# Kernel optimization log

Measured on AMD Instinct MI355X. Metric: run time of the kernel, lower is better.

## Reference

```python
import jax, jax.numpy as jnp
import numpy as np

N_NODES = 50000
N_EDGES = 800000
IN_DIM = 128
OUT_DIM = 256


def setup_inputs() -> dict:
    key = jax.random.key(0)
    k1, k2, k3, k4 = jax.random.split(key, 4)
    feat = jax.random.normal(k1, (N_NODES, IN_DIM), dtype=jnp.float32)
    # xavier_uniform with relu gain, shape [in_dim, out_dim] (applied as h @ W)
    gain = np.sqrt(2.0)
    bound = gain * np.sqrt(6.0 / (IN_DIM + OUT_DIM))
    W = jax.random.uniform(k2, (IN_DIM, OUT_DIM), dtype=jnp.float32,
                           minval=-bound, maxval=bound)
    src = jax.random.randint(k3, (N_EDGES,), 0, N_NODES, dtype=jnp.int64)
    dst = jax.random.randint(k4, (N_EDGES,), 0, N_NODES, dtype=jnp.int64)
    return {"feat": feat, "W": W, "src": src, "dst": dst}


def reference(feat, W, src, dst):
    n = feat.shape[0]
    # mean aggregation over incoming neighbors (copy_src + mean on dst)
    msg_sum = jax.ops.segment_sum(feat[src], dst, num_segments=n)  # [N, in_dim]
    deg = jax.ops.segment_sum(jnp.ones_like(dst, dtype=feat.dtype), dst,
                              num_segments=n)  # [N]
    h_neigh = msg_sum / jnp.maximum(deg, 1.0)[:, None]  # zero-degree -> 0
    # self_loop=False path: fc((feat + h_neigh) / 2), then relu
    h = ((feat + h_neigh) * 0.5) @ W  # [N, out_dim]
    return jax.nn.relu(h)
```

## Files before the change

kernel.cpp:

```cpp
#include <hip/hip_runtime.h>
#include <hip/hip_fp16.h>

#define N_NODES 50000
#define N_EDGES 800000
#define IN_DIM  128
#define OUT_DIM 256
#define SCAN_BLOCKS ((N_NODES + 255) / 256)
#define WT_STRIDE 136

typedef _Float16 f16x8 __attribute__((ext_vector_type(8)));
typedef float f32x4 __attribute__((ext_vector_type(4)));

__device__ __forceinline__ int detect_i64(const int* __restrict__ idx) {
  int orv = 0;
#pragma unroll
  for (int j = 1; j < 32; j += 2) orv |= idx[j];
  return orv == 0;
}

__global__ __launch_bounds__(256) void hist_cast(
    const int* __restrict__ dst, const float* __restrict__ feat,
    __half* __restrict__ feat16, int* __restrict__ hist,
    int* __restrict__ slot) {
  const int f = detect_i64(dst);
  const int e = blockIdx.x * 256 + threadIdx.x;
  const int d = dst[f ? 2 * (long)e : (long)e];
  slot[e] = atomicAdd(&hist[d], 1);

  if (feat16 != nullptr) {
    size_t i = (size_t)e * 8;
    float4 v0 = *reinterpret_cast<const float4*>(feat + i);
    float4 v1 = *reinterpret_cast<const float4*>(feat + i + 4);
    __half2 h[4];
    h[0] = __floats2half2_rn(v0.x, v0.y);
    h[1] = __floats2half2_rn(v0.z, v0.w);
    h[2] = __floats2half2_rn(v1.x, v1.y);
    h[3] = __floats2half2_rn(v1.z, v1.w);
    *reinterpret_cast<float4*>(feat16 + i) = *reinterpret_cast<float4*>(h);
  }
}

__global__ __launch_bounds__(256) void scan_block(
    const int* __restrict__ hist, int* __restrict__ row_start,
    int* __restrict__ bsum, const float* __restrict__ W,
    __half* __restrict__ WT16g) {
  __shared__ int s[256];
  int tid = threadIdx.x;
  int i = blockIdx.x * 256 + tid;
  int v = (i < N_NODES) ? hist[i] : 0;
  s[tid] = v;
  __syncthreads();
  for (int off = 1; off < 256; off <<= 1) {
    int t = (tid >= off) ? s[tid - off] : 0;
    __syncthreads();
    s[tid] += t;
    __syncthreads();
  }
  if (i < N_NODES) row_start[i] = s[tid] - v;
  if (tid == 255) bsum[blockIdx.x] = s[255];

  if (blockIdx.x < 128) {
    int n = 2 * blockIdx.x + (tid >> 7);
    int k = tid & 127;
    WT16g[n * IN_DIM + k] = __float2half(W[k * OUT_DIM + n]);
  }
}

__global__ __launch_bounds__(256) void scan_add(
    const int* __restrict__ bsum, int* __restrict__ row_start) {
  __shared__ int sb[256];
  int tid = threadIdx.x;
  sb[tid] = (tid < (int)blockIdx.x) ? bsum[tid] : 0;
  __syncthreads();
  for (int off = 128; off > 0; off >>= 1) {
    if (tid < off) sb[tid] += sb[tid + off];
    __syncthreads();
  }
  int i = blockIdx.x * 256 + tid;
  if (i < N_NODES) row_start[i] += sb[0];
  if (i == 0) row_start[N_NODES] = N_EDGES;
}

__global__ __launch_bounds__(256) void scatter_kernel(
    const int* __restrict__ src, const int* __restrict__ dst,
    const int* __restrict__ row_start, const int* __restrict__ slot,
    int* __restrict__ esrc) {
  const int f = detect_i64(src);
  const int t = blockIdx.x * 256 + threadIdx.x;
  if (t >= N_EDGES / 2) return;
  int s0, s1, d0, d1;
  if (f) {
    int4 sv = *reinterpret_cast<const int4*>(src + 4 * (long)t);
    int4 dv = *reinterpret_cast<const int4*>(dst + 4 * (long)t);
    s0 = sv.x; s1 = sv.z; d0 = dv.x; d1 = dv.z;
  } else {
    int2 sv = *reinterpret_cast<const int2*>(src + 2 * (long)t);
    int2 dv = *reinterpret_cast<const int2*>(dst + 2 * (long)t);
    s0 = sv.x; s1 = sv.y; d0 = dv.x; d1 = dv.y;
  }
  int2 sl = *reinterpret_cast<const int2*>(slot + 2 * (long)t);
  esrc[row_start[d0] + sl.x] = s0;
  esrc[row_start[d1] + sl.y] = s1;
}

__global__ __launch_bounds__(256) void aggregate_f16(
    const float* __restrict__ feat, const __half* __restrict__ feat16,
    const int* __restrict__ esrc, const int* __restrict__ row_start,
    __half2* __restrict__ x) {
  int node = blockIdx.x * 4 + ((int)threadIdx.x >> 6);
  int lane = (int)threadIdx.x & 63;
  if (node >= N_NODES) return;
  int rs = row_start[node];
  int re = row_start[node + 1];
  float2 a0 = {0.f, 0.f}, a1 = {0.f, 0.f}, a2 = {0.f, 0.f}, a3 = {0.f, 0.f};
  int e = rs;
  for (; e + 3 < re; e += 4) {
    int s0 = esrc[e + 0];
    int s1 = esrc[e + 1];
    int s2 = esrc[e + 2];
    int s3 = esrc[e + 3];
    float2 v0 = __half22float2(*reinterpret_cast<const __half2*>(
        feat16 + (size_t)s0 * IN_DIM + lane * 2));
    float2 v1 = __half22float2(*reinterpret_cast<const __half2*>(
        feat16 + (size_t)s1 * IN_DIM + lane * 2));
    float2 v2 = __half22float2(*reinterpret_cast<const __half2*>(
        feat16 + (size_t)s2 * IN_DIM + lane * 2));
    float2 v3 = __half22float2(*reinterpret_cast<const __half2*>(
        feat16 + (size_t)s3 * IN_DIM + lane * 2));
    a0.x += v0.x; a0.y += v0.y;
    a1.x += v1.x; a1.y += v1.y;
    a2.x += v2.x; a2.y += v2.y;
    a3.x += v3.x; a3.y += v3.y;
  }
  for (; e < re; ++e) {
    float2 v0 = __half22float2(*reinterpret_cast<const __half2*>(
        feat16 + (size_t)esrc[e] * IN_DIM + lane * 2));
    a0.x += v0.x; a0.y += v0.y;
  }
  float deg = (float)(re - rs);
  float rdeg = (deg > 0.f) ? 1.0f / deg : 0.0f;
  float2 f = *reinterpret_cast<const float2*>(
      feat + (size_t)node * IN_DIM + lane * 2);
  float x0 = (f.x + ((a0.x + a1.x) + (a2.x + a3.x)) * rdeg) * 0.5f;
  float x1 = (f.y + ((a0.y + a1.y) + (a2.y + a3.y)) * rdeg) * 0.5f;
  x[(size_t)node * (IN_DIM / 2) + lane] = __floats2half2_rn(x0, x1);
}

__global__ __launch_bounds__(256) void aggregate_f32(
    const float* __restrict__ feat, const int* __restrict__ esrc,
    const int* __restrict__ row_start, __half2* __restrict__ x) {
  int node = blockIdx.x * 4 + ((int)threadIdx.x >> 6);
  int lane = (int)threadIdx.x & 63;
  if (node >= N_NODES) return;
  int rs = row_start[node];
  int re = row_start[node + 1];
  float2 a0 = {0.f, 0.f}, a1 = {0.f, 0.f};
  int e = rs;
  for (; e + 1 < re; e += 2) {
    float2 v0 = *reinterpret_cast<const float2*>(
        feat + (size_t)esrc[e] * IN_DIM + lane * 2);
    float2 v1 = *reinterpret_cast<const float2*>(
        feat + (size_t)esrc[e + 1] * IN_DIM + lane * 2);
    a0.x += v0.x; a0.y += v0.y;
    a1.x += v1.x; a1.y += v1.y;
  }
  if (e < re) {
    float2 v0 = *reinterpret_cast<const float2*>(
        feat + (size_t)esrc[e] * IN_DIM + lane * 2);
    a0.x += v0.x; a0.y += v0.y;
  }
  float deg = (float)(re - rs);
  float rdeg = (deg > 0.f) ? 1.0f / deg : 0.0f;
  float2 f = *reinterpret_cast<const float2*>(
      feat + (size_t)node * IN_DIM + lane * 2);
  float x0 = (f.x + (a0.x + a1.x) * rdeg) * 0.5f;
  float x1 = (f.y + (a0.y + a1.y) * rdeg) * 0.5f;
  x[(size_t)node * (IN_DIM / 2) + lane] = __floats2half2_rn(x0, x1);
}

__global__ __launch_bounds__(256) void mfma_gemm(
    const _Float16* __restrict__ x, const __half* __restrict__ WT16g,
    float* __restrict__ out) {
  __shared__ _Float16 WT[OUT_DIM * WT_STRIDE];

  const int tid = threadIdx.x;
#pragma unroll
  for (int i = 0; i < 16; ++i) {
    int c = i * 256 + tid;
    int n = c >> 4;
    int kc = c & 15;
    *reinterpret_cast<float4*>(&WT[n * WT_STRIDE + kc * 8]) =
        *reinterpret_cast<const float4*>(WT16g + c * 8);
  }
  __syncthreads();

  const int wave = tid >> 6;
  const int lane = tid & 63;
  const int m = lane & 15;
  const int g = lane >> 4;
  const long row_base = (long)blockIdx.x * 128 + wave * 32;

  f16x8 a[2][4];
#pragma unroll
  for (int rt = 0; rt < 2; ++rt) {
    long row = row_base + rt * 16 + m;
#pragma unroll
    for (int kt = 0; kt < 4; ++kt) {
      if (row < N_NODES) {
        a[rt][kt] = *reinterpret_cast<const f16x8*>(
            x + row * IN_DIM + kt * 32 + g * 8);
      } else {
        a[rt][kt] = f16x8{};
      }
    }
  }

#pragma unroll
  for (int nt = 0; nt < 16; ++nt) {
    f16x8 b[4];
#pragma unroll
    for (int kt = 0; kt < 4; ++kt) {
      b[kt] = *reinterpret_cast<const f16x8*>(
          &WT[(nt * 16 + m) * WT_STRIDE + kt * 32 + g * 8]);
    }
    f32x4 acc0 = {0.f, 0.f, 0.f, 0.f};
    f32x4 acc1 = {0.f, 0.f, 0.f, 0.f};
#pragma unroll
    for (int kt = 0; kt < 4; ++kt) {
      acc0 = __builtin_amdgcn_mfma_f32_16x16x32_f16(a[0][kt], b[kt], acc0, 0, 0, 0);
      acc1 = __builtin_amdgcn_mfma_f32_16x16x32_f16(a[1][kt], b[kt], acc1, 0, 0, 0);
    }
    const int col = nt * 16 + m;
#pragma unroll
    for (int j = 0; j < 4; ++j) {
      long r0 = row_base + g * 4 + j;
      long r1 = row_base + 16 + g * 4 + j;
      if (r0 < N_NODES)
        __builtin_nontemporal_store(fmaxf(acc0[j], 0.f),
                                    &out[r0 * OUT_DIM + col]);
      if (r1 < N_NODES)
        __builtin_nontemporal_store(fmaxf(acc1[j], 0.f),
                                    &out[r1 * OUT_DIM + col]);
    }
  }
}

extern "C" void kernel_launch(void* const* d_in, const int* in_sizes, int n_in,
                              void* d_out, int out_size, void* d_ws,
                              size_t ws_size, hipStream_t stream) {
  const float* feat = (const float*)d_in[0];
  const float* W = (const float*)d_in[1];
  const int* src = (const int*)d_in[2];
  const int* dst = (const int*)d_in[3];
  float* out = (float*)d_out;

  char* p = (char*)d_ws;
  __half* x = (__half*)p;    p += (size_t)N_NODES * IN_DIM * 2;
  int* slot = (int*)x;
  int* esrc = (int*)p;       p += (size_t)N_EDGES * 4;
  int* hist = (int*)p;       p += (size_t)N_NODES * 4;
  int* row_start = (int*)p;  p += (size_t)(N_NODES + 1) * 4;
  int* bsum = (int*)p;       p += 256 * 4;
  p = (char*)(((uintptr_t)p + 15) & ~(uintptr_t)15);
  __half* WT16g = (__half*)p; p += (size_t)OUT_DIM * IN_DIM * 2;
  __half* feat16 = (__half*)p;
  size_t need_f16 =
      ((char*)feat16 - (char*)d_ws) + (size_t)N_NODES * IN_DIM * 2;
  const bool f16_path = (ws_size >= need_f16);

  hipMemsetAsync(hist, 0, (size_t)N_NODES * 4, stream);

  const int eblocks = N_EDGES / 256;
  hist_cast<<<eblocks, 256, 0, stream>>>(dst, feat,
                                         f16_path ? feat16 : nullptr, hist,
                                         slot);
  scan_block<<<SCAN_BLOCKS, 256, 0, stream>>>(hist, row_start, bsum, W, WT16g);
  scan_add<<<SCAN_BLOCKS, 256, 0, stream>>>(bsum, row_start);
  scatter_kernel<<<(N_EDGES / 2 + 255) / 256, 256, 0, stream>>>(
      src, dst, row_start, slot, esrc);
  if (f16_path) {
    aggregate_f16<<<(N_NODES + 3) / 4, 256, 0, stream>>>(feat, feat16, esrc,
                                                         row_start,
                                                         (__half2*)x);
  } else {
    aggregate_f32<<<(N_NODES + 3) / 4, 256, 0, stream>>>(feat, esrc, row_start,
                                                         (__half2*)x);
  }
  mfma_gemm<<<(N_NODES + 127) / 128, 256, 0, stream>>>(
      (const _Float16*)x, WT16g, out);
}
```

Baseline: 201.1 us.

## Fuse CSR build stages into one persistent kernel with grid barriers

Replaces the histogram/cast, two-pass scan and scatter kernels with a single persistent 1024-block kernel that uses software grid barriers between phases. The block scan is redone over 49 nodes per block so each block handles its own slice. The aim is to remove several kernel launch gaps and drain points. It also drops the fp32 fallback aggregation path. The grid barrier relies on all 1024 blocks being co-resident, which can deadlock if occupancy is lower, and spinning barriers add their own latency.

```diff
diff --git a/kernel.cpp b/kernel.cpp
--- a/kernel.cpp
+++ b/kernel.cpp
@@ -5,8 +5,9 @@
 #define N_EDGES 800000
 #define IN_DIM  128
 #define OUT_DIM 256
-#define SCAN_BLOCKS ((N_NODES + 255) / 256)
 #define WT_STRIDE 136
+#define NBLK 1024
+#define NODES_PER_BLK 49
 
 typedef _Float16 f16x8 __attribute__((ext_vector_type(8)));
 typedef float f32x4 __attribute__((ext_vector_type(4)));
@@ -18,17 +19,42 @@
   return orv == 0;
 }
 
-__global__ __launch_bounds__(256) void hist_cast(
-    const int* __restrict__ dst, const float* __restrict__ feat,
-    __half* __restrict__ feat16, int* __restrict__ hist,
-    int* __restrict__ slot) {
-  const int f = detect_i64(dst);
-  const int e = blockIdx.x * 256 + threadIdx.x;
-  const int d = dst[f ? 2 * (long)e : (long)e];
-  slot[e] = atomicAdd(&hist[d], 1);
-
-  if (feat16 != nullptr) {
-    size_t i = (size_t)e * 8;
+__device__ __forceinline__ void grid_barrier(int* counter, int* gen) {
+  __syncthreads();
+  if (threadIdx.x == 0) {
+    __threadfence();
+    int g = __hip_atomic_load(gen, __ATOMIC_RELAXED, __HIP_MEMORY_SCOPE_AGENT);
+    int prev = __hip_atomic_fetch_add(counter, 1, __ATOMIC_ACQ_REL,
+                                      __HIP_MEMORY_SCOPE_AGENT);
+    if (prev == NBLK - 1) {
+      __hip_atomic_store(counter, 0, __ATOMIC_RELAXED,
+                         __HIP_MEMORY_SCOPE_AGENT);
+      __hip_atomic_store(gen, g + 1, __ATOMIC_RELEASE,
+                         __HIP_MEMORY_SCOPE_AGENT);
+    } else {
+      while (__hip_atomic_load(gen, __ATOMIC_ACQUIRE,
+                               __HIP_MEMORY_SCOPE_AGENT) == g) {
+        __builtin_amdgcn_s_sleep(2);
+      }
+    }
+  }
+  __syncthreads();
+}
+
+__global__ __launch_bounds__(256, 4) void mega_csr(
+    const float* __restrict__ feat, const float* __restrict__ W,
+    const int* __restrict__ src, const int* __restrict__ dst,
+    __half* __restrict__ feat16, __half* __restrict__ WT16g,
+    int* __restrict__ hist, int* __restrict__ slot,
+    int* __restrict__ row_start, int* __restrict__ bsum,
+    int* __restrict__ esrc, int* __restrict__ bar) {
+  const int tid = threadIdx.x;
+  const int b = blockIdx.x;
+  const int gtid = b * 256 + tid;
+  const int fd = detect_i64(dst);
+
+  for (int t = gtid; t < (N_NODES * IN_DIM) / 8; t += NBLK * 256) {
+    size_t i = (size_t)t * 8;
     float4 v0 = *reinterpret_cast<const float4*>(feat + i);
     float4 v1 = *reinterpret_cast<const float4*>(feat + i + 4);
     __half2 h[4];
@@ -38,69 +64,70 @@
     h[3] = __floats2half2_rn(v1.z, v1.w);
     *reinterpret_cast<float4*>(feat16 + i) = *reinterpret_cast<float4*>(h);
   }
-}
-
-__global__ __launch_bounds__(256) void scan_block(
-    const int* __restrict__ hist, int* __restrict__ row_start,
-    int* __restrict__ bsum, const float* __restrict__ W,
-    __half* __restrict__ WT16g) {
-  __shared__ int s[256];
-  int tid = threadIdx.x;
-  int i = blockIdx.x * 256 + tid;
-  int v = (i < N_NODES) ? hist[i] : 0;
-  s[tid] = v;
-  __syncthreads();
-  for (int off = 1; off < 256; off <<= 1) {
-    int t = (tid >= off) ? s[tid - off] : 0;
+  if (gtid < OUT_DIM * IN_DIM) {
+    int k = gtid & (IN_DIM - 1);
+    int n = gtid >> 7;
+    WT16g[gtid] = __float2half(W[k * OUT_DIM + n]);
+  }
+  for (int e = gtid; e < N_EDGES; e += NBLK * 256) {
+    int d = dst[fd ? 2 * (long)e : (long)e];
+    slot[e] = atomicAdd(&hist[d], 1);
+  }
+
+  grid_barrier(bar, bar + 1);
+
+  __shared__ int s[64];
+  __shared__ int sb[256];
+  int v = 0;
+  if (tid < 64) {
+    int node = b * NODES_PER_BLK + tid;
+    v = (tid < NODES_PER_BLK && node < N_NODES) ? hist[node] : 0;
+    s[tid] = v;
+  }
+  __syncthreads();
+  for (int off = 1; off < 64; off <<= 1) {
+    int t2 = (tid < 64 && tid >= off) ? s[tid - off] : 0;
     __syncthreads();
-    s[tid] += t;
+    if (tid < 64) s[tid] += t2;
     __syncthreads();
   }
-  if (i < N_NODES) row_start[i] = s[tid] - v;
-  if (tid == 255) bsum[blockIdx.x] = s[255];
-
-  if (blockIdx.x < 128) {
-    int n = 2 * blockIdx.x + (tid >> 7);
-    int k = tid & 127;
-    WT16g[n * IN_DIM + k] = __float2half(W[k * OUT_DIM + n]);
-  }
-}
-
-__global__ __launch_bounds__(256) void scan_add(
-    const int* __restrict__ bsum, int* __restrict__ row_start) {
-  __shared__ int sb[256];
-  int tid = threadIdx.x;
-  sb[tid] = (tid < (int)blockIdx.x) ? bsum[tid] : 0;
+  if (tid == 0) bsum[b] = s[NODES_PER_BLK - 1];
+
+  grid_barrier(bar, bar + 1);
+
+  int part = 0;
+  for (int i = tid; i < b; i += 256) part += bsum[i];
+  sb[tid] = part;
   __syncthreads();
   for (int off = 128; off > 0; off >>= 1) {
     if (tid < off) sb[tid] += sb[tid + off];
     __syncthreads();
   }
-  int i = blockIdx.x * 256 + tid;
-  if (i < N_NODES) row_start[i] += sb[0];
-  if (i == 0) row_start[N_NODES] = N_EDGES;
-}
-
-__global__ __launch_bounds__(256) void scatter_kernel(
-    const int* __restrict__ src, const int* __restrict__ dst,
-    const int* __restrict__ row_start, const int* __restrict__ slot,
-    int* __restrict__ esrc) {
-  const int f = detect_i64(src);
-  const int t = blockIdx.x * 256 + threadIdx.x;
-  if (t >= N_EDGES / 2) return;
-  int s0, s1, d0, d1;
-  if (f) {
-    int4 sv = *reinterpret_cast<const int4*>(src + 4 * (long)t);
-    int4 dv = *reinterpret_cast<const int4*>(dst + 4 * (long)t);
-    s0 = sv.x; s1 = sv.z; d0 = dv.x; d1 = dv.z;
-  } else {
-    int2 sv = *reinterpret_cast<const int2*>(src + 2 * (long)t);
-    int2 dv = *reinterpret_cast<const int2*>(dst + 2 * (long)t);
-    s0 = sv.x; s1 = sv.y; d0 = dv.x; d1 = dv.y;
-  }
-  int2 sl = *reinterpret_cast<const int2*>(slot + 2 * (long)t);
-  esrc[row_start[d0] + sl.x] = s0;
-  esrc[row_start[d1] + sl.y] = s1;
+  int offset = sb[0];
+  if (tid < NODES_PER_BLK) {
+    int node = b * NODES_PER_BLK + tid;
+    if (node < N_NODES) row_start[node] = (s[tid] - v) + offset;
+  }
+  if (gtid == 0) row_start[N_NODES] = N_EDGES;
+
+  grid_barrier(bar, bar + 1);
+
+  const int fs = detect_i64(src);
+  for (int t = gtid; t < N_EDGES / 2; t += NBLK * 256) {
+    int s0, s1, d0, d1;
+    if (fs) {
+      int4 sv = *reinterpret_cast<const int4*>(src + 4 * (long)t);
+      int4 dv = *reinterpret_cast<const int4*>(dst + 4 * (long)t);
+      s0 = sv.x; s1 = sv.z; d0 = dv.x; d1 = dv.z;
+    } else {
+      int2 sv = *reinterpret_cast<const int2*>(src + 2 * (long)t);
+      int2 dv = *reinterpret_cast<const int2*>(dst + 2 * (long)t);
+      s0 = sv.x; s1 = sv.y; d0 = dv.x; d1 = dv.y;
+    }
+    int2 sl = *reinterpret_cast<const int2*>(slot + 2 * (long)t);
+    esrc[row_start[d0] + sl.x] = s0;
+    esrc[row_start[d1] + sl.y] = s1;
+  }
 }
 
 __global__ __launch_bounds__(256) void aggregate_f16(
@@ -146,38 +173,6 @@
   x[(size_t)node * (IN_DIM / 2) + lane] = __floats2half2_rn(x0, x1);
 }
 
-__global__ __launch_bounds__(256) void aggregate_f32(
-    const float* __restrict__ feat, const int* __restrict__ esrc,
-    const int* __restrict__ row_start, __half2* __restrict__ x) {
-  int node = blockIdx.x * 4 + ((int)threadIdx.x >> 6);
-  int lane = (int)threadIdx.x & 63;
-  if (node >= N_NODES) return;
-  int rs = row_start[node];
-  int re = row_start[node + 1];
-  float2 a0 = {0.f, 0.f}, a1 = {0.f, 0.f};
-  int e = rs;
-  for (; e + 1 < re; e += 2) {
-    float2 v0 = *reinterpret_cast<const float2*>(
-        feat + (size_t)esrc[e] * IN_DIM + lane * 2);
-    float2 v1 = *reinterpret_cast<const float2*>(
-        feat + (size_t)esrc[e + 1] * IN_DIM + lane * 2);
-    a0.x += v0.x; a0.y += v0.y;
-    a1.x += v1.x; a1.y += v1.y;
-  }
-  if (e < re) {
-    float2 v0 = *reinterpret_cast<const float2*>(
-        feat + (size_t)esrc[e] * IN_DIM + lane * 2);
-    a0.x += v0.x; a0.y += v0.y;
-  }
-  float deg = (float)(re - rs);
-  float rdeg = (deg > 0.f) ? 1.0f / deg : 0.0f;
-  float2 f = *reinterpret_cast<const float2*>(
-      feat + (size_t)node * IN_DIM + lane * 2);
-  float x0 = (f.x + (a0.x + a1.x) * rdeg) * 0.5f;
-  float x1 = (f.y + (a0.y + a1.y) * rdeg) * 0.5f;
-  x[(size_t)node * (IN_DIM / 2) + lane] = __floats2half2_rn(x0, x1);
-}
-
 __global__ __launch_bounds__(256) void mfma_gemm(
     const _Float16* __restrict__ x, const __half* __restrict__ WT16g,
     float* __restrict__ out) {
@@ -217,18 +212,18 @@
 
 #pragma unroll
   for (int nt = 0; nt < 16; ++nt) {
-    f16x8 b[4];
+    f16x8 bfr[4];
 #pragma unroll
     for (int kt = 0; kt < 4; ++kt) {
-      b[kt] = *reinterpret_cast<const f16x8*>(
+      bfr[kt] = *reinterpret_cast<const f16x8*>(
           &WT[(nt * 16 + m) * WT_STRIDE + kt * 32 + g * 8]);
     }
     f32x4 acc0 = {0.f, 0.f, 0.f, 0.f};
     f32x4 acc1 = {0.f, 0.f, 0.f, 0.f};
 #pragma unroll
     for (int kt = 0; kt < 4; ++kt) {
-      acc0 = __builtin_amdgcn_mfma_f32_16x16x32_f16(a[0][kt], b[kt], acc0, 0, 0, 0);
-      acc1 = __builtin_amdgcn_mfma_f32_16x16x32_f16(a[1][kt], b[kt], acc1, 0, 0, 0);
+      acc0 = __builtin_amdgcn_mfma_f32_16x16x32_f16(a[0][kt], bfr[kt], acc0, 0, 0, 0);
+      acc1 = __builtin_amdgcn_mfma_f32_16x16x32_f16(a[1][kt], bfr[kt], acc1, 0, 0, 0);
     }
     const int col = nt * 16 + m;
 #pragma unroll
@@ -259,33 +254,19 @@
   int* slot = (int*)x;
   int* esrc = (int*)p;       p += (size_t)N_EDGES * 4;
   int* hist = (int*)p;       p += (size_t)N_NODES * 4;
+  int* bar = (int*)p;        p += 16;
   int* row_start = (int*)p;  p += (size_t)(N_NODES + 1) * 4;
-  int* bsum = (int*)p;       p += 256 * 4;
+  int* bsum = (int*)p;       p += (size_t)NBLK * 4;
   p = (char*)(((uintptr_t)p + 15) & ~(uintptr_t)15);
   __half* WT16g = (__half*)p; p += (size_t)OUT_DIM * IN_DIM * 2;
   __half* feat16 = (__half*)p;
-  size_t need_f16 =
-      ((char*)feat16 - (char*)d_ws) + (size_t)N_NODES * IN_DIM * 2;
-  const bool f16_path = (ws_size >= need_f16);
-
-  hipMemsetAsync(hist, 0, (size_t)N_NODES * 4, stream);
-
-  const int eblocks = N_EDGES / 256;
-  hist_cast<<<eblocks, 256, 0, stream>>>(dst, feat,
-                                         f16_path ? feat16 : nullptr, hist,
-                                         slot);
-  scan_block<<<SCAN_BLOCKS, 256, 0, stream>>>(hist, row_start, bsum, W, WT16g);
-  scan_add<<<SCAN_BLOCKS, 256, 0, stream>>>(bsum, row_start);
-  scatter_kernel<<<(N_EDGES / 2 + 255) / 256, 256, 0, stream>>>(
-      src, dst, row_start, slot, esrc);
-  if (f16_path) {
-    aggregate_f16<<<(N_NODES + 3) / 4, 256, 0, stream>>>(feat, feat16, esrc,
-                                                         row_start,
-                                                         (__half2*)x);
-  } else {
-    aggregate_f32<<<(N_NODES + 3) / 4, 256, 0, stream>>>(feat, esrc, row_start,
-                                                         (__half2*)x);
-  }
+
+  hipMemsetAsync(hist, 0, (size_t)N_NODES * 4 + 16, stream);
+
+  mega_csr<<<NBLK, 256, 0, stream>>>(feat, W, src, dst, feat16, WT16g, hist,
+                                     slot, row_start, bsum, esrc, bar);
+  aggregate_f16<<<(N_NODES + 3) / 4, 256, 0, stream>>>(feat, feat16, esrc,
+                                                       row_start, (__half2*)x);
   mfma_gemm<<<(N_NODES + 127) / 128, 256, 0, stream>>>(
       (const _Float16*)x, WT16g, out);
 }
```

New measurement: 542.3 us. 170% more time.
